# Performance work log

Hardware: AMD Instinct MI355X
Metric: run time of the kernel (lower is better)

Reference implementation:

```python
import jax, jax.numpy as jnp
import numpy as np

EPS = 1e-12  # torch F.normalize eps


def setup_inputs() -> dict:
    key = jax.random.key(0)
    k1, k2, k3 = jax.random.split(key, 3)
    N, D, L = 8192, 768, 24576
    x = jax.random.normal(k1, (N, D), dtype=jnp.float32)
    # paper init: row-normalized gaussian rows of shape [latent_dim, input_dim]
    w = jax.random.normal(k2, (L, D), dtype=jnp.float32)
    enc_w = w / jnp.maximum(jnp.linalg.norm(w, axis=1, keepdims=True), EPS)
    enc_b = jax.random.normal(k3, (L,), dtype=jnp.float32) * 0.01
    pre_bias = jnp.zeros((D,), dtype=jnp.float32)
    return {"x": x, "enc_w": enc_w, "enc_b": enc_b, "pre_bias": pre_bias, "k": 32}


def _topk_mask(latents, k):
    # keep values >= k-th largest per row (ties kept, as in the torch code)
    vals, _ = jax.lax.top_k(latents, k)            # [N, k]
    thresh = vals[:, -1:]                          # [N, 1]
    return latents * (latents >= thresh)


def reference(x, enc_w, enc_b, pre_bias, k):
    # norm_input: subtract pre_bias then L2-normalize rows
    xc = x - pre_bias
    xn = xc / jnp.maximum(jnp.linalg.norm(xc, axis=1, keepdims=True), EPS)
    latents = xn @ enc_w.T + enc_b                 # [N, L]
    sparse = _topk_mask(latents, k)                # [N, L], ~k nonzeros/row
    # tied decoder: F.linear(sparse, enc_w.t()) == sparse @ enc_w
    out = sparse @ enc_w + pre_bias                # [N, D]
    return out, sparse
```

## Files before the change

### kernel.cpp

```cpp
#include <hip/hip_runtime.h>
#include <hip/hip_bf16.h>
#include <stdint.h>

#define N_ROWS 8192
#define DIM    768
#define LAT    24576
#define KSEL   32

using bf16x8 = __attribute__((ext_vector_type(8))) short;
using f32x4  = __attribute__((ext_vector_type(4))) float;

__device__ __forceinline__ unsigned short f2bf(float f) {
  unsigned int b = __float_as_uint(f);
  return (unsigned short)((b + 0x7FFFu + ((b >> 16) & 1u)) >> 16);
}
__device__ __forceinline__ float bf2f(unsigned short u) {
  return __uint_as_float(((unsigned int)u) << 16);
}
__device__ __forceinline__ unsigned int mapf(float f) {
  unsigned int u = __float_as_uint(f);
  return (u & 0x80000000u) ? ~u : (u | 0x80000000u);
}

__device__ __forceinline__ void gload16(const unsigned short* g, unsigned short* l) {
  __builtin_amdgcn_global_load_lds(
      (const __attribute__((address_space(1))) unsigned int*)(uintptr_t)g,
      (__attribute__((address_space(3))) unsigned int*)(unsigned int)(uintptr_t)l,
      16, 0, 0);
}

__global__ __launch_bounds__(192) void k_norm(const float* __restrict__ x,
                                              const float* __restrict__ pre_bias,
                                              float* __restrict__ xn,
                                              unsigned short* __restrict__ xnbf) {
  const int row = blockIdx.x;
  const int t   = threadIdx.x;
  float4 xc = *(const float4*)&x[(size_t)row * DIM + t * 4];
  float4 pb = *(const float4*)&pre_bias[t * 4];
  xc.x -= pb.x; xc.y -= pb.y; xc.z -= pb.z; xc.w -= pb.w;
  double ss = (double)xc.x * xc.x + (double)xc.y * xc.y
            + (double)xc.z * xc.z + (double)xc.w * xc.w;
  #pragma unroll
  for (int off = 32; off; off >>= 1) ss += __shfl_down(ss, off);
  __shared__ double wsum[3];
  if ((t & 63) == 0) wsum[t >> 6] = ss;
  __syncthreads();
  const double tot = wsum[0] + wsum[1] + wsum[2];
  const float nrm = (float)fmax(sqrt(tot), 1e-12);
  float4 o;
  o.x = xc.x / nrm; o.y = xc.y / nrm; o.z = xc.z / nrm; o.w = xc.w / nrm;
  *(float4*)&xn[(size_t)row * DIM + t * 4] = o;
  if (xnbf) {
    ushort4 h;
    h.x = f2bf(o.x); h.y = f2bf(o.y); h.z = f2bf(o.z); h.w = f2bf(o.w);
    *(ushort4*)&xnbf[(size_t)row * DIM + t * 4] = h;
  }
}

__global__ __launch_bounds__(256) void k_cvt(const float* __restrict__ W,
                                             unsigned short* __restrict__ Wbf) {
  const int n4 = LAT * DIM / 4;
  const int stride = gridDim.x * blockDim.x;
  for (int i = blockIdx.x * blockDim.x + threadIdx.x; i < n4; i += stride) {
    float4 v = *(const float4*)&W[(size_t)i * 4];
    ushort4 h;
    h.x = f2bf(v.x); h.y = f2bf(v.y); h.z = f2bf(v.z); h.w = f2bf(v.w);
    *(ushort4*)&Wbf[(size_t)i * 4] = h;
  }
}

__global__ __launch_bounds__(256) void k_gemm_bf16(const unsigned short* __restrict__ A,
                                                   const unsigned short* __restrict__ B,
                                                   const float* __restrict__ bias,
                                                   unsigned short* __restrict__ C) {
  __shared__ __align__(16) unsigned short Al[2][128 * 32];
  __shared__ __align__(16) unsigned short Bl[2][128 * 32];
  const int tid  = threadIdx.x;
  const int lane = tid & 63;
  const int wave = tid >> 6;
  const int bm = blockIdx.y * 128;
  const int bn = blockIdx.x * 128;
  const int wr = (wave >> 1) * 64;
  const int wc = (wave & 1) * 64;
  const int fr = lane & 15;
  const int fq = lane >> 4;

  const int seg0 = wave * 2;
  const int rseg = lane >> 2;
  const int ch   = lane & 3;

  const unsigned short* gA0 = &A[(size_t)(bm + 16 * seg0 +      rseg) * DIM + ch * 8];
  const unsigned short* gA1 = &A[(size_t)(bm + 16 * seg0 + 16 + rseg) * DIM + ch * 8];
  const unsigned short* gB0 = &B[(size_t)(bn + 16 * seg0 +      rseg) * DIM + ch * 8];
  const unsigned short* gB1 = &B[(size_t)(bn + 16 * seg0 + 16 + rseg) * DIM + ch * 8];

  f32x4 acc[4][4];
  #pragma unroll
  for (int m = 0; m < 4; ++m)
    #pragma unroll
    for (int n = 0; n < 4; ++n) acc[m][n] = (f32x4){0.f, 0.f, 0.f, 0.f};

#define STAGE(buf, k0)                                            \
  do {                                                            \
    gload16(gA0 + (k0), &Al[buf][(seg0)     * 512]);              \
    gload16(gA1 + (k0), &Al[buf][(seg0 + 1) * 512]);              \
    gload16(gB0 + (k0), &Bl[buf][(seg0)     * 512]);              \
    gload16(gB1 + (k0), &Bl[buf][(seg0 + 1) * 512]);              \
  } while (0)

  STAGE(0, 0);

  const int NT = DIM / 32;
  for (int kt = 0; kt < NT; ++kt) {
    const int buf = kt & 1;
    __syncthreads();
    if (kt + 1 < NT) STAGE(buf ^ 1, (kt + 1) * 32);
    bf16x8 af[4], bfr[4];
    #pragma unroll
    for (int m = 0; m < 4; ++m)
      af[m] = *(const bf16x8*)&Al[buf][(wr + m * 16 + fr) * 32 + fq * 8];
    #pragma unroll
    for (int n = 0; n < 4; ++n)
      bfr[n] = *(const bf16x8*)&Bl[buf][(wc + n * 16 + fr) * 32 + fq * 8];
    #pragma unroll
    for (int m = 0; m < 4; ++m)
      #pragma unroll
      for (int n = 0; n < 4; ++n)
        acc[m][n] = __builtin_amdgcn_mfma_f32_16x16x32_bf16(af[m], bfr[n], acc[m][n], 0, 0, 0);
  }
#undef STAGE

  #pragma unroll
  for (int n = 0; n < 4; ++n) {
    const int col = bn + wc + n * 16 + fr;
    const float bv = bias[col];
    #pragma unroll
    for (int m = 0; m < 4; ++m) {
      #pragma unroll
      for (int j = 0; j < 4; ++j) {
        const int row = bm + wr + m * 16 + fq * 4 + j;
        C[(size_t)row * LAT + col] = f2bf(acc[m][n][j] + bv);
      }
    }
  }
}

#define NBINS 8192
#define MARGIN 8e-3f
#define CCAP 192

__global__ __launch_bounds__(512) void k_screen(const unsigned short* __restrict__ S,
                                                int* __restrict__ cand_idx,
                                                int* __restrict__ cand_cnt) {
  const int row = blockIdx.x;
  const int t   = threadIdx.x;
  const unsigned short* rp = S + (size_t)row * LAT;

  float v[48];
  #pragma unroll
  for (int i = 0; i < 12; ++i) {
    ushort4 h = *(const ushort4*)&rp[(i * 512 + t) * 4];
    v[i * 4 + 0] = bf2f(h.x); v[i * 4 + 1] = bf2f(h.y);
    v[i * 4 + 2] = bf2f(h.z); v[i * 4 + 3] = bf2f(h.w);
  }

  __shared__ unsigned int hist[NBINS];
  __shared__ unsigned int csum[512];
  __shared__ unsigned int sh_chunk, sh_rchunk, sh_thru;
  __shared__ int sh_nc;
  if (t == 0) sh_nc = 0;
  #pragma unroll
  for (int i = 0; i < NBINS / 512; ++i) hist[t + i * 512] = 0u;
  __syncthreads();

  #pragma unroll
  for (int i = 0; i < 48; ++i) atomicAdd(&hist[mapf(v[i]) >> 19], 1u);
  __syncthreads();

  unsigned int cs = 0;
  #pragma unroll
  for (int i = 0; i < 16; ++i) cs += hist[t * 16 + i];
  csum[t] = cs;
  __syncthreads();
  for (int off = 1; off < 512; off <<= 1) {
    unsigned int add = (t + off < 512) ? csum[t + off] : 0u;
    __syncthreads();
    csum[t] += add;
    __syncthreads();
  }
  {
    const unsigned int nxt = (t + 1 < 512) ? csum[t + 1] : 0u;
    if (csum[t] >= KSEL && nxt < KSEL) { sh_chunk = (unsigned)t; sh_rchunk = nxt; }
  }
  __syncthreads();
  if (t == 0) {
    const unsigned int c0 = sh_chunk * 16u;
    unsigned int cum = sh_rchunk;
    unsigned int bin = c0;
    for (int b = 15; b >= 0; --b) {
      const unsigned int h = hist[c0 + b];
      if (cum + h >= KSEL) { bin = c0 + b; break; }
      cum += h;
    }
    const unsigned int lo = bin << 19;
    const unsigned int orig = (lo & 0x80000000u) ? (lo & 0x7FFFFFFFu) : ~lo;
    const float L = __uint_as_float(orig);
    sh_thru = mapf(L - MARGIN);
  }
  __syncthreads();
  const unsigned int thru = sh_thru;

  #pragma unroll
  for (int i = 0; i < 48; ++i) {
    if (mapf(v[i]) >= thru) {
      int p = atomicAdd(&sh_nc, 1);
      if (p < CCAP) cand_idx[row * CCAP + p] = ((i >> 2) * 512 + t) * 4 + (i & 3);
    }
  }
  __syncthreads();
  if (t == 0) cand_cnt[row] = (sh_nc < CCAP) ? sh_nc : CCAP;
}

__global__ __launch_bounds__(256) void k_rescore_seq(const float* __restrict__ xn,
                                                     const float* __restrict__ W,
                                                     const float* __restrict__ bias,
                                                     const int* __restrict__ cand_idx,
                                                     const int* __restrict__ cand_cnt,
                                                     float* __restrict__ tk_val,
                                                     int* __restrict__ tk_idx,
                                                     int* __restrict__ tk_cnt) {
  const int row = blockIdx.x;
  const int t   = threadIdx.x;
  const int cnt = cand_cnt[row];

  __shared__ float xs[DIM];
  __shared__ float rv[CCAP];
  __shared__ unsigned int sh_t;
  __shared__ int sh_kc;
  if (t == 0) sh_kc = 0;
  if (t < 192) *(float4*)&xs[t * 4] = *(const float4*)&xn[(size_t)row * DIM + t * 4];
  __syncthreads();

  if (t < cnt) {
    const int idx = cand_idx[row * CCAP + t];
    const float* wp = &W[(size_t)idx * DIM];
    float acc = 0.0f;
    for (int k4 = 0; k4 < DIM / 4; ++k4) {
      const float4 wv = *(const float4*)&wp[k4 * 4];
      acc = fmaf(xs[k4 * 4 + 0], wv.x, acc);
      acc = fmaf(xs[k4 * 4 + 1], wv.y, acc);
      acc = fmaf(xs[k4 * 4 + 2], wv.z, acc);
      acc = fmaf(xs[k4 * 4 + 3], wv.w, acc);
    }
    rv[t] = acc + bias[idx];
  }
  __syncthreads();

  if (t < cnt) {
    const unsigned int uj = mapf(rv[t]);
    unsigned int g = 0, ge = 0;
    for (int i = 0; i < cnt; ++i) {
      const unsigned int ui = mapf(rv[i]);
      g  += (ui >  uj);
      ge += (ui >= uj);
    }
    if (g < KSEL && ge >= KSEL) sh_t = uj;
  }
  __syncthreads();
  if (t < cnt) {
    const float val = rv[t];
    if (mapf(val) >= sh_t) {
      int p = atomicAdd(&sh_kc, 1);
      if (p < 64) { tk_val[row * 64 + p] = val; tk_idx[row * 64 + p] = cand_idx[row * CCAP + t]; }
    }
  }
  __syncthreads();
  if (t == 0) tk_cnt[row] = (sh_kc < 64) ? sh_kc : 64;
}

__global__ __launch_bounds__(256) void k_scatter_dec(const float* __restrict__ tk_val,
                                                     const int* __restrict__ tk_idx,
                                                     const int* __restrict__ tk_cnt,
                                                     const float* __restrict__ W,
                                                     const float* __restrict__ pre_bias,
                                                     float* __restrict__ sparse,
                                                     float* __restrict__ out) {
  const int row = blockIdx.x;
  const int t   = threadIdx.x;
  float* rp = sparse + (size_t)row * LAT;
  const float4 z = {0.f, 0.f, 0.f, 0.f};
  #pragma unroll
  for (int i = 0; i < LAT / (256 * 4); ++i) *(float4*)&rp[(i * 256 + t) * 4] = z;
  __syncthreads();
  const int cnt = tk_cnt[row];
  if (t < cnt) rp[tk_idx[row * 64 + t]] = tk_val[row * 64 + t];
  if (t < 192) {
    float4 acc = *(const float4*)&pre_bias[t * 4];
    for (int e = 0; e < cnt; ++e) {
      const float val = tk_val[row * 64 + e];
      const int   idx = tk_idx[row * 64 + e];
      const float4 w = *(const float4*)&W[(size_t)idx * DIM + t * 4];
      acc.x = fmaf(val, w.x, acc.x);
      acc.y = fmaf(val, w.y, acc.y);
      acc.z = fmaf(val, w.z, acc.z);
      acc.w = fmaf(val, w.w, acc.w);
    }
    *(float4*)&out[(size_t)row * DIM + t * 4] = acc;
  }
}

#define BM 128
#define BN 128
#define BK 32
#define PAD 4

__global__ __launch_bounds__(256) void k_gemm(const float* __restrict__ A,
                                              const float* __restrict__ B,
                                              const float* __restrict__ bias,
                                              float* __restrict__ C) {
  __shared__ float As[BK][BM + PAD];
  __shared__ float Bs[BK][BN + PAD];
  const int tid = threadIdx.x;
  const int bm = blockIdx.y * BM;
  const int bn = blockIdx.x * BN;
  const int tx = tid & 15;
  const int ty = tid >> 4;
  const int kq = tid & 7;
  const int rr = tid >> 3;

  float acc[8][8];
  #pragma unroll
  for (int i = 0; i < 8; ++i)
    #pragma unroll
    for (int j = 0; j < 8; ++j) acc[i][j] = 0.0f;

  float4 va[4], vb[4];
  #pragma unroll
  for (int i = 0; i < 4; ++i) {
    const int row = rr + 32 * i;
    va[i] = *(const float4*)&A[(size_t)(bm + row) * DIM + kq * 4];
    vb[i] = *(const float4*)&B[(size_t)(bn + row) * DIM + kq * 4];
  }

  for (int k0 = 0; k0 < DIM; k0 += BK) {
    #pragma unroll
    for (int i = 0; i < 4; ++i) {
      const int row = rr + 32 * i;
      As[kq * 4 + 0][row] = va[i].x; As[kq * 4 + 1][row] = va[i].y;
      As[kq * 4 + 2][row] = va[i].z; As[kq * 4 + 3][row] = va[i].w;
      Bs[kq * 4 + 0][row] = vb[i].x; Bs[kq * 4 + 1][row] = vb[i].y;
      Bs[kq * 4 + 2][row] = vb[i].z; Bs[kq * 4 + 3][row] = vb[i].w;
    }
    __syncthreads();
    if (k0 + BK < DIM) {
      #pragma unroll
      for (int i = 0; i < 4; ++i) {
        const int row = rr + 32 * i;
        va[i] = *(const float4*)&A[(size_t)(bm + row) * DIM + (k0 + BK) + kq * 4];
        vb[i] = *(const float4*)&B[(size_t)(bn + row) * DIM + (k0 + BK) + kq * 4];
      }
    }
    #pragma unroll
    for (int k = 0; k < BK; ++k) {
      float a[8], b[8];
      *(float4*)&b[0] = *(const float4*)&Bs[k][tx * 4];
      *(float4*)&b[4] = *(const float4*)&Bs[k][64 + tx * 4];
      *(float4*)&a[0] = *(const float4*)&As[k][ty * 8];
      *(float4*)&a[4] = *(const float4*)&As[k][ty * 8 + 4];
      #pragma unroll
      for (int i = 0; i < 8; ++i)
        #pragma unroll
        for (int j = 0; j < 8; ++j)
          acc[i][j] = fmaf(a[i], b[j], acc[i][j]);
    }
    __syncthreads();
  }

  const float4 b0 = *(const float4*)&bias[bn + tx * 4];
  const float4 b1 = *(const float4*)&bias[bn + 64 + tx * 4];
  #pragma unroll
  for (int i = 0; i < 8; ++i) {
    const size_t m = (size_t)(bm + ty * 8 + i);
    float4 v0, v1;
    v0.x = acc[i][0] + b0.x; v0.y = acc[i][1] + b0.y;
    v0.z = acc[i][2] + b0.z; v0.w = acc[i][3] + b0.w;
    v1.x = acc[i][4] + b1.x; v1.y = acc[i][5] + b1.y;
    v1.z = acc[i][6] + b1.z; v1.w = acc[i][7] + b1.w;
    *(float4*)&C[m * LAT + bn + tx * 4]      = v0;
    *(float4*)&C[m * LAT + bn + 64 + tx * 4] = v1;
  }
}

#define TPB_TK 512
#define CAND_CAP 512

template <int EMIT>
__global__ __launch_bounds__(TPB_TK) void k_topk(float* __restrict__ lat,
                                                 float* __restrict__ tk_val,
                                                 int* __restrict__ tk_idx,
                                                 int* __restrict__ tk_cnt) {
  const int row = blockIdx.x;
  const int t   = threadIdx.x;
  float* rowp = lat + (size_t)row * LAT;

  float4 v[12];
  #pragma unroll
  for (int i = 0; i < 12; ++i) v[i] = *(const float4*)&rowp[(i * TPB_TK + t) * 4];

  __shared__ unsigned int hist[NBINS];
  __shared__ unsigned int csum[TPB_TK];
  __shared__ unsigned int cand[CAND_CAP];
  __shared__ int sh_nc, sh_kc;
  __shared__ unsigned int sh_bin, sh_need, sh_thresh, sh_rchunk, sh_chunk;

  if (t == 0) { sh_nc = 0; sh_kc = 0; }
  #pragma unroll
  for (int i = 0; i < NBINS / TPB_TK; ++i) hist[t + i * TPB_TK] = 0u;
  __syncthreads();

  #pragma unroll
  for (int i = 0; i < 12; ++i) {
    atomicAdd(&hist[mapf(v[i].x) >> 19], 1u);
    atomicAdd(&hist[mapf(v[i].y) >> 19], 1u);
    atomicAdd(&hist[mapf(v[i].z) >> 19], 1u);
    atomicAdd(&hist[mapf(v[i].w) >> 19], 1u);
  }
  __syncthreads();

  unsigned int cs = 0;
  #pragma unroll
  for (int i = 0; i < 16; ++i) cs += hist[t * 16 + i];
  csum[t] = cs;
  __syncthreads();
  for (int off = 1; off < TPB_TK; off <<= 1) {
    unsigned int add = (t + off < TPB_TK) ? csum[t + off] : 0u;
    __syncthreads();
    csum[t] += add;
    __syncthreads();
  }
  {
    const unsigned int nxt = (t + 1 < TPB_TK) ? csum[t + 1] : 0u;
    if (csum[t] >= KSEL && nxt < KSEL) { sh_chunk = (unsigned)t; sh_rchunk = nxt; }
  }
  __syncthreads();
  if (t == 0) {
    const unsigned int c0 = sh_chunk * 16u;
    unsigned int cum = sh_rchunk;
    for (int b = 15; b >= 0; --b) {
      const unsigned int h = hist[c0 + b];
      if (cum + h >= KSEL) { sh_bin = c0 + b; sh_need = KSEL - cum; break; }
      cum += h;
    }
  }
  __syncthreads();
  const unsigned int bstar = sh_bin;

  #pragma unroll
  for (int i = 0; i < 12; ++i) {
    unsigned int u;
    u = mapf(v[i].x); if ((u >> 19) == bstar) { int p = atomicAdd(&sh_nc, 1); if (p < CAND_CAP) cand[p] = u; }
    u = mapf(v[i].y); if ((u >> 19) == bstar) { int p = atomicAdd(&sh_nc, 1); if (p < CAND_CAP) cand[p] = u; }
    u = mapf(v[i].z); if ((u >> 19) == bstar) { int p = atomicAdd(&sh_nc, 1); if (p < CAND_CAP) cand[p] = u; }
    u = mapf(v[i].w); if ((u >> 19) == bstar) { int p = atomicAdd(&sh_nc, 1); if (p < CAND_CAP) cand[p] = u; }
  }
  __syncthreads();
  const int nc = (sh_nc < CAND_CAP) ? sh_nc : CAND_CAP;
  const unsigned int need = sh_need;
  for (int j = t; j < nc; j += TPB_TK) {
    const unsigned int uj = cand[j];
    unsigned int g = 0, ge = 0;
    for (int i = 0; i < nc; ++i) {
      g  += (cand[i] >  uj);
      ge += (cand[i] >= uj);
    }
    if (g < need && ge >= need) sh_thresh = uj;
  }
  __syncthreads();
  const unsigned int tu = sh_thresh;

  #pragma unroll
  for (int i = 0; i < 12; ++i) {
    const int base = (i * TPB_TK + t) * 4;
    float4 o = v[i];
    unsigned int u;
    u = mapf(o.x); if (u >= tu) { if (EMIT) { int p = atomicAdd(&sh_kc, 1); if (p < 64) { tk_val[row * 64 + p] = o.x; tk_idx[row * 64 + p] = base + 0; } } } else o.x = 0.0f;
    u = mapf(o.y); if (u >= tu) { if (EMIT) { int p = atomicAdd(&sh_kc, 1); if (p < 64) { tk_val[row * 64 + p] = o.y; tk_idx[row * 64 + p] = base + 1; } } } else o.y = 0.0f;
    u = mapf(o.z); if (u >= tu) { if (EMIT) { int p = atomicAdd(&sh_kc, 1); if (p < 64) { tk_val[row * 64 + p] = o.z; tk_idx[row * 64 + p] = base + 2; } } } else o.z = 0.0f;
    u = mapf(o.w); if (u >= tu) { if (EMIT) { int p = atomicAdd(&sh_kc, 1); if (p < 64) { tk_val[row * 64 + p] = o.w; tk_idx[row * 64 + p] = base + 3; } } } else o.w = 0.0f;
    *(float4*)&rowp[base] = o;
  }
  if (EMIT) {
    __syncthreads();
    if (t == 0) tk_cnt[row] = (sh_kc < 64) ? sh_kc : 64;
  }
}

__global__ __launch_bounds__(192) void k_dec(const float* __restrict__ tk_val,
                                             const int* __restrict__ tk_idx,
                                             const int* __restrict__ tk_cnt,
                                             const float* __restrict__ W,
                                             const float* __restrict__ pre_bias,
                                             float* __restrict__ out) {
  const int row = blockIdx.x;
  const int t   = threadIdx.x;
  const int cnt = tk_cnt[row];
  float4 acc = *(const float4*)&pre_bias[t * 4];
  for (int e = 0; e < cnt; ++e) {
    const float val = tk_val[row * 64 + e];
    const int   idx = tk_idx[row * 64 + e];
    const float4 w = *(const float4*)&W[(size_t)idx * DIM + t * 4];
    acc.x = fmaf(val, w.x, acc.x);
    acc.y = fmaf(val, w.y, acc.y);
    acc.z = fmaf(val, w.z, acc.z);
    acc.w = fmaf(val, w.w, acc.w);
  }
  *(float4*)&out[(size_t)row * DIM + t * 4] = acc;
}

__global__ __launch_bounds__(256) void k_dec_scan(const float* __restrict__ sparse,
                                                  const float* __restrict__ W,
                                                  const float* __restrict__ pre_bias,
                                                  float* __restrict__ out) {
  const int row = blockIdx.x;
  const int t   = threadIdx.x;
  const float* rowp = sparse + (size_t)row * LAT;

  __shared__ float sval[96];
  __shared__ int   sidx[96];
  __shared__ int   scnt;
  if (t == 0) scnt = 0;
  __syncthreads();

  #pragma unroll
  for (int i = 0; i < LAT / (256 * 4); ++i) {
    const int base = (i * 256 + t) * 4;
    const float4 v = *(const float4*)&rowp[base];
    if (v.x != 0.0f) { int p = atomicAdd(&scnt, 1); if (p < 96) { sval[p] = v.x; sidx[p] = base + 0; } }
    if (v.y != 0.0f) { int p = atomicAdd(&scnt, 1); if (p < 96) { sval[p] = v.y; sidx[p] = base + 1; } }
    if (v.z != 0.0f) { int p = atomicAdd(&scnt, 1); if (p < 96) { sval[p] = v.z; sidx[p] = base + 2; } }
    if (v.w != 0.0f) { int p = atomicAdd(&scnt, 1); if (p < 96) { sval[p] = v.w; sidx[p] = base + 3; } }
  }
  __syncthreads();
  const int cnt = (scnt < 96) ? scnt : 96;

  if (t < 192) {
    float4 acc = *(const float4*)&pre_bias[t * 4];
    for (int e = 0; e < cnt; ++e) {
      const float val = sval[e];
      const float4 w = *(const float4*)&W[(size_t)sidx[e] * DIM + t * 4];
      acc.x = fmaf(val, w.x, acc.x);
      acc.y = fmaf(val, w.y, acc.y);
      acc.z = fmaf(val, w.z, acc.z);
      acc.w = fmaf(val, w.w, acc.w);
    }
    *(float4*)&out[(size_t)row * DIM + t * 4] = acc;
  }
}

extern "C" void kernel_launch(void* const* d_in, const int* in_sizes, int n_in,
                              void* d_out, int out_size, void* d_ws, size_t ws_size,
                              hipStream_t stream) {
  const float* x        = (const float*)d_in[0];
  const float* enc_w    = (const float*)d_in[1];
  const float* enc_b    = (const float*)d_in[2];
  const float* pre_bias = (const float*)d_in[3];

  float* out    = (float*)d_out;
  float* sparse = (float*)d_out + (size_t)N_ROWS * DIM;
  float* xn     = out;

  char* spb = (char*)sparse;
  unsigned short* xnbf   = (unsigned short*)spb;
  unsigned short* wbf    = (unsigned short*)(spb + (size_t)N_ROWS * DIM * 2);
  unsigned short* screen = (unsigned short*)(sparse + (size_t)N_ROWS * LAT / 2);

  char* wsb = (char*)d_ws;
  size_t off = 0;
  int*   cand_idx = (int*)(wsb + off); off += (size_t)N_ROWS * CCAP * 4;
  int*   cand_cnt = (int*)(wsb + off); off += (size_t)N_ROWS * 4;
  float* tk_val   = (float*)(wsb + off); off += (size_t)N_ROWS * 64 * 4;
  int*   tk_idx   = (int*)(wsb + off); off += (size_t)N_ROWS * 64 * 4;
  int*   tk_cnt   = (int*)(wsb + off); off += (size_t)N_ROWS * 4;
  const bool fast = ws_size >= off;

  if (fast) {
    k_norm<<<N_ROWS, 192, 0, stream>>>(x, pre_bias, xn, xnbf);
    k_cvt<<<2048, 256, 0, stream>>>(enc_w, wbf);
    dim3 ggrid(LAT / 128, N_ROWS / 128);
    k_gemm_bf16<<<ggrid, 256, 0, stream>>>(xnbf, wbf, enc_b, screen);
    k_screen<<<N_ROWS, 512, 0, stream>>>(screen, cand_idx, cand_cnt);
    k_rescore_seq<<<N_ROWS, 256, 0, stream>>>(xn, enc_w, enc_b, cand_idx, cand_cnt,
                                              tk_val, tk_idx, tk_cnt);
    k_scatter_dec<<<N_ROWS, 256, 0, stream>>>(tk_val, tk_idx, tk_cnt, enc_w, pre_bias,
                                              sparse, out);
  } else {
    const size_t ws_small = (size_t)N_ROWS * 64 * 4 * 2 + (size_t)N_ROWS * 4;
    const bool use_lists = ws_size >= ws_small;
    float* f_val = (float*)d_ws;
    int*   f_idx = (int*)(f_val + (size_t)N_ROWS * 64);
    int*   f_cnt = f_idx + (size_t)N_ROWS * 64;

    k_norm<<<N_ROWS, 192, 0, stream>>>(x, pre_bias, xn, nullptr);
    dim3 ggrid(LAT / BN, N_ROWS / BM);
    k_gemm<<<ggrid, 256, 0, stream>>>(xn, enc_w, enc_b, sparse);
    if (use_lists) {
      k_topk<1><<<N_ROWS, TPB_TK, 0, stream>>>(sparse, f_val, f_idx, f_cnt);
      k_dec<<<N_ROWS, 192, 0, stream>>>(f_val, f_idx, f_cnt, enc_w, pre_bias, out);
    } else {
      k_topk<0><<<N_ROWS, TPB_TK, 0, stream>>>(sparse, nullptr, nullptr, nullptr);
      k_dec_scan<<<N_ROWS, 256, 0, stream>>>(sparse, enc_w, pre_bias, out);
    }
  }
}
```

Baseline: 1.810 ms.

## Stage GEMM epilogue through LDS, radix-select threshold, nontemporal zero stores

Three separate changes. The bf16 GEMM epilogue now writes its tile into shared memory and then issues coalesced 16-byte nontemporal stores, replacing scattered 2-byte global writes. The screening kernel drops its 8192-bin shared histogram and prefix scan and finds the threshold with a 16-step bitwise radix search that counts via wave shuffles and block reductions. The sparse output zero-fill now uses nontemporal stores. The radix search adds 16 block barriers per row and repeated passes over 48 registers.

```diff
diff --git a/kernel.cpp b/kernel.cpp
--- a/kernel.cpp
+++ b/kernel.cpp
@@ -9,6 +9,7 @@
 
 using bf16x8 = __attribute__((ext_vector_type(8))) short;
 using f32x4  = __attribute__((ext_vector_type(4))) float;
+using u32x4  = __attribute__((ext_vector_type(4))) unsigned int;
 
 __device__ __forceinline__ unsigned short f2bf(float f) {
   unsigned int b = __float_as_uint(f);
@@ -73,8 +74,7 @@
                                                    const unsigned short* __restrict__ B,
                                                    const float* __restrict__ bias,
                                                    unsigned short* __restrict__ C) {
-  __shared__ __align__(16) unsigned short Al[2][128 * 32];
-  __shared__ __align__(16) unsigned short Bl[2][128 * 32];
+  __shared__ __align__(16) unsigned short smem[2][2][128 * 32];
   const int tid  = threadIdx.x;
   const int lane = tid & 63;
   const int wave = tid >> 6;
@@ -102,10 +102,10 @@
 
 #define STAGE(buf, k0)                                            \
   do {                                                            \
-    gload16(gA0 + (k0), &Al[buf][(seg0)     * 512]);              \
-    gload16(gA1 + (k0), &Al[buf][(seg0 + 1) * 512]);              \
-    gload16(gB0 + (k0), &Bl[buf][(seg0)     * 512]);              \
-    gload16(gB1 + (k0), &Bl[buf][(seg0 + 1) * 512]);              \
+    gload16(gA0 + (k0), &smem[0][buf][(seg0)     * 512]);         \
+    gload16(gA1 + (k0), &smem[0][buf][(seg0 + 1) * 512]);         \
+    gload16(gB0 + (k0), &smem[1][buf][(seg0)     * 512]);         \
+    gload16(gB1 + (k0), &smem[1][buf][(seg0 + 1) * 512]);         \
   } while (0)
 
   STAGE(0, 0);
@@ -118,10 +118,10 @@
     bf16x8 af[4], bfr[4];
     #pragma unroll
     for (int m = 0; m < 4; ++m)
-      af[m] = *(const bf16x8*)&Al[buf][(wr + m * 16 + fr) * 32 + fq * 8];
+      af[m] = *(const bf16x8*)&smem[0][buf][(wr + m * 16 + fr) * 32 + fq * 8];
     #pragma unroll
     for (int n = 0; n < 4; ++n)
-      bfr[n] = *(const bf16x8*)&Bl[buf][(wc + n * 16 + fr) * 32 + fq * 8];
+      bfr[n] = *(const bf16x8*)&smem[1][buf][(wc + n * 16 + fr) * 32 + fq * 8];
     #pragma unroll
     for (int m = 0; m < 4; ++m)
       #pragma unroll
@@ -130,22 +130,33 @@
   }
 #undef STAGE
 
+  __syncthreads();
+  unsigned short* Cl = &smem[0][0][0];
   #pragma unroll
   for (int n = 0; n < 4; ++n) {
-    const int col = bn + wc + n * 16 + fr;
-    const float bv = bias[col];
+    const int col = wc + n * 16 + fr;
+    const float bv = bias[bn + col];
     #pragma unroll
     for (int m = 0; m < 4; ++m) {
       #pragma unroll
       for (int j = 0; j < 4; ++j) {
-        const int row = bm + wr + m * 16 + fq * 4 + j;
-        C[(size_t)row * LAT + col] = f2bf(acc[m][n][j] + bv);
+        const int row = wr + m * 16 + fq * 4 + j;
+        Cl[row * 128 + col] = f2bf(acc[m][n][j] + bv);
       }
     }
   }
-}
-
-#define NBINS 8192
+  __syncthreads();
+  #pragma unroll
+  for (int i = 0; i < 8; ++i) {
+    const int c   = i * 256 + tid;
+    const int row = c >> 4;
+    const int cc  = c & 15;
+    const u32x4 v = *(const u32x4*)&Cl[c * 8];
+    __builtin_nontemporal_store(v,
+        (u32x4*)&C[(size_t)(bm + row) * LAT + bn + cc * 8]);
+  }
+}
+
 #define MARGIN 8e-3f
 #define CCAP 192
 
@@ -156,63 +167,43 @@
   const int t   = threadIdx.x;
   const unsigned short* rp = S + (size_t)row * LAT;
 
-  float v[48];
+  unsigned int u[48];
   #pragma unroll
   for (int i = 0; i < 12; ++i) {
     ushort4 h = *(const ushort4*)&rp[(i * 512 + t) * 4];
-    v[i * 4 + 0] = bf2f(h.x); v[i * 4 + 1] = bf2f(h.y);
-    v[i * 4 + 2] = bf2f(h.z); v[i * 4 + 3] = bf2f(h.w);
-  }
-
-  __shared__ unsigned int hist[NBINS];
-  __shared__ unsigned int csum[512];
-  __shared__ unsigned int sh_chunk, sh_rchunk, sh_thru;
+    u[i * 4 + 0] = mapf(bf2f(h.x));
+    u[i * 4 + 1] = mapf(bf2f(h.y));
+    u[i * 4 + 2] = mapf(bf2f(h.z));
+    u[i * 4 + 3] = mapf(bf2f(h.w));
+  }
+
+  __shared__ unsigned int wcnt[8];
   __shared__ int sh_nc;
   if (t == 0) sh_nc = 0;
-  #pragma unroll
-  for (int i = 0; i < NBINS / 512; ++i) hist[t + i * 512] = 0u;
-  __syncthreads();
-
-  #pragma unroll
-  for (int i = 0; i < 48; ++i) atomicAdd(&hist[mapf(v[i]) >> 19], 1u);
-  __syncthreads();
-
-  unsigned int cs = 0;
-  #pragma unroll
-  for (int i = 0; i < 16; ++i) cs += hist[t * 16 + i];
-  csum[t] = cs;
-  __syncthreads();
-  for (int off = 1; off < 512; off <<= 1) {
-    unsigned int add = (t + off < 512) ? csum[t + off] : 0u;
-    __syncthreads();
-    csum[t] += add;
-    __syncthreads();
-  }
-  {
-    const unsigned int nxt = (t + 1 < 512) ? csum[t + 1] : 0u;
-    if (csum[t] >= KSEL && nxt < KSEL) { sh_chunk = (unsigned)t; sh_rchunk = nxt; }
-  }
-  __syncthreads();
-  if (t == 0) {
-    const unsigned int c0 = sh_chunk * 16u;
-    unsigned int cum = sh_rchunk;
-    unsigned int bin = c0;
-    for (int b = 15; b >= 0; --b) {
-      const unsigned int h = hist[c0 + b];
-      if (cum + h >= KSEL) { bin = c0 + b; break; }
-      cum += h;
-    }
-    const unsigned int lo = bin << 19;
-    const unsigned int orig = (lo & 0x80000000u) ? (lo & 0x7FFFFFFFu) : ~lo;
-    const float L = __uint_as_float(orig);
-    sh_thru = mapf(L - MARGIN);
-  }
-  __syncthreads();
-  const unsigned int thru = sh_thru;
+
+  unsigned int T = 0u;
+  #pragma unroll 1
+  for (int b = 31; b >= 16; --b) {
+    const unsigned int Tc = T | (1u << b);
+    unsigned int c = 0;
+    #pragma unroll
+    for (int i = 0; i < 48; ++i) c += (u[i] >= Tc) ? 1u : 0u;
+    #pragma unroll
+    for (int off = 32; off; off >>= 1) c += __shfl_down(c, off);
+    if ((t & 63) == 0) wcnt[t >> 6] = c;
+    __syncthreads();
+    unsigned int tot = wcnt[0] + wcnt[1] + wcnt[2] + wcnt[3]
+                     + wcnt[4] + wcnt[5] + wcnt[6] + wcnt[7];
+    if (tot >= KSEL) T = Tc;
+    __syncthreads();
+  }
+  const unsigned int orig = (T & 0x80000000u) ? (T & 0x7FFFFFFFu) : ~T;
+  const float v32 = __uint_as_float(orig);
+  const unsigned int thru = mapf(v32 - MARGIN);
 
   #pragma unroll
   for (int i = 0; i < 48; ++i) {
-    if (mapf(v[i]) >= thru) {
+    if (u[i] >= thru) {
       int p = atomicAdd(&sh_nc, 1);
       if (p < CCAP) cand_idx[row * CCAP + p] = ((i >> 2) * 512 + t) * 4 + (i & 3);
     }
@@ -288,9 +279,10 @@
   const int row = blockIdx.x;
   const int t   = threadIdx.x;
   float* rp = sparse + (size_t)row * LAT;
-  const float4 z = {0.f, 0.f, 0.f, 0.f};
-  #pragma unroll
-  for (int i = 0; i < LAT / (256 * 4); ++i) *(float4*)&rp[(i * 256 + t) * 4] = z;
+  const f32x4 z = {0.f, 0.f, 0.f, 0.f};
+  #pragma unroll
+  for (int i = 0; i < LAT / (256 * 4); ++i)
+    __builtin_nontemporal_store(z, (f32x4*)&rp[(i * 256 + t) * 4]);
   __syncthreads();
   const int cnt = tk_cnt[row];
   if (t < cnt) rp[tk_idx[row * 64 + t]] = tk_val[row * 64 + t];
@@ -313,6 +305,7 @@
 #define BN 128
 #define BK 32
 #define PAD 4
+#define NBINS 8192
 
 __global__ __launch_bounds__(256) void k_gemm(const float* __restrict__ A,
                                               const float* __restrict__ B,
```

After: 1.826 ms. No clear change (+0.9%).
